# Performance work log

Measured on AMD Instinct MI355X. Metric: run time of the kernel, lower is better.

Reference implementation:

```python
import jax, jax.numpy as jnp
import numpy as np

B, T, D_MODEL, H, DH = 4, 2048, 768, 12, 64


def _rope_tables(T, dh):
    # standard rotary frequencies, (T, dh//2)
    inv_freq = 1.0 / (10000.0 ** (np.arange(0, dh, 2, dtype=np.float32) / dh))
    t = np.arange(T, dtype=np.float32)
    ang = np.outer(t, inv_freq)  # (T, dh//2)
    return jnp.asarray(np.cos(ang)), jnp.asarray(np.sin(ang))


def setup_inputs() -> dict:
    key = jax.random.key(0)
    ks = jax.random.split(key, 5)
    scale = 1.0 / np.sqrt(D_MODEL)
    x = jax.random.normal(ks[0], (B, T, D_MODEL), dtype=jnp.float32)
    wq = jax.random.normal(ks[1], (D_MODEL, D_MODEL), dtype=jnp.float32) * scale
    wk = jax.random.normal(ks[2], (D_MODEL, D_MODEL), dtype=jnp.float32) * scale
    wv = jax.random.normal(ks[3], (D_MODEL, D_MODEL), dtype=jnp.float32) * scale
    wo = jax.random.normal(ks[4], (D_MODEL, D_MODEL), dtype=jnp.float32) * scale
    rope_cos, rope_sin = _rope_tables(T, DH)
    return {"x": x, "rope_cos": rope_cos, "rope_sin": rope_sin,
            "wq": wq, "wk": wk, "wv": wv, "wo": wo}


def _apply_rope(x, cos, sin):
    # x: (B, H, T, DH), cos/sin: (T, DH//2) -> interleaved rotation
    t = x.shape[2]
    c = cos[:t][None, None]  # (1,1,T,DH//2)
    s = sin[:t][None, None]
    x1 = x[..., ::2]
    x2 = x[..., 1::2]
    return jnp.stack([x1 * c - x2 * s, x1 * s + x2 * c], axis=-1).reshape(x.shape)


def reference(x, rope_cos, rope_sin, wq, wk, wv, wo):
    b, t, _ = x.shape
    # Linear (torch nn.Linear: y = x @ W.T), split heads -> (B,H,T,DH)
    q = (x @ wq.T).reshape(b, t, H, DH).transpose(0, 2, 1, 3)
    k = (x @ wk.T).reshape(b, t, H, DH).transpose(0, 2, 1, 3)
    v = (x @ wv.T).reshape(b, t, H, DH).transpose(0, 2, 1, 3)
    q = _apply_rope(q, rope_cos, rope_sin)
    k = _apply_rope(k, rope_cos, rope_sin)
    scores = jnp.einsum("bhqd,bhkd->bhqk", q, k) * (DH ** -0.5)
    causal = jnp.tril(jnp.ones((t, t), dtype=bool))  # (T,T)
    scores = jnp.where(causal[None, None], scores, -jnp.inf)
    attn = jax.nn.softmax(scores, axis=-1)
    out = jnp.einsum("bhqk,bhkd->bhqd", attn, v)
    out = out.transpose(0, 2, 1, 3).reshape(b, t, H * DH)
    return out @ wo.T
```

## Files before the change

kernel.cpp:

```cpp
#include <hip/hip_runtime.h>
#include <hip/hip_bf16.h>
#include <math.h>

#define B_ 4
#define T_ 2048
#define DM 768
#define H_ 12
#define DH 64

typedef __attribute__((ext_vector_type(4))) float f32x4;
typedef __attribute__((ext_vector_type(8))) short s16x8;

typedef const __attribute__((address_space(1))) void* gas1_t;
typedef __attribute__((address_space(3))) void* las3_t;

__device__ __forceinline__ ushort f2b(float f) {
  union { float f; unsigned u; } v; v.f = f;
  unsigned u = v.u;
  u += 0x7fffu + ((u >> 16) & 1u);
  return (ushort)(u >> 16);
}
__device__ __forceinline__ float b2f(ushort b) {
  union { unsigned u; float f; } v; v.u = ((unsigned)b) << 16;
  return v.f;
}
__device__ __forceinline__ unsigned cvt_pk_bf16(float lo, float hi) {
  unsigned r;
  asm("v_cvt_pk_bf16_f32 %0, %1, %2" : "=v"(r) : "v"(lo), "v"(hi));
  return r;
}

__global__ void cvt_all(const float* __restrict__ x,
                        const float* __restrict__ wq, const float* __restrict__ wk,
                        const float* __restrict__ wv, const float* __restrict__ wo,
                        const float* __restrict__ rc, const float* __restrict__ rs,
                        ushort* __restrict__ xb, ushort* __restrict__ wqkv,
                        ushort* __restrict__ wob, float2* __restrict__ cs2) {
  const int bid = blockIdx.x, t = threadIdx.x;
  if (bid < 6144) {
    int i = bid * 256 + t;
    float4 v = ((const float4*)x)[i];
    ushort4 o;
    o.x = f2b(v.x); o.y = f2b(v.y); o.z = f2b(v.z); o.w = f2b(v.w);
    ((ushort4*)xb)[i] = o;
  } else if (bid < 8448) {
    int i = (bid - 6144) * 256 + t;
    int which = i / 147456, j = i - which * 147456;
    const float* src = which == 0 ? wq : which == 1 ? wk : which == 2 ? wv : wo;
    ushort* dst = which < 3 ? wqkv + (size_t)which * 589824 : wob;
    float4 v = ((const float4*)src)[j];
    ushort4 o;
    o.x = f2b(v.x); o.y = f2b(v.y); o.z = f2b(v.z); o.w = f2b(v.w);
    ((ushort4*)dst)[j] = o;
  } else {
    int i = (bid - 8448) * 256 + t;
    cs2[i] = make_float2(rc[i], rs[i]);
  }
}

__global__ __launch_bounds__(256, 3) void gemm_qkv(
    const ushort* __restrict__ A, const ushort* __restrict__ Bw,
    const float2* __restrict__ cs2,
    ushort* __restrict__ Qb, ushort* __restrict__ Kb, ushort* __restrict__ Vt) {
  const int K = 768;
  __shared__ ushort As[128 * 64];
  __shared__ ushort Bs[128 * 64];
  const int bid = blockIdx.x;
  const int xcd = bid & 7;
  const int jj = bid >> 3;
  const int mloc = jj / 18, nn0 = jj - mloc * 18;
  const int m0 = (xcd * 8 + mloc) * 128, n0 = nn0 * 128;
  const int tid = threadIdx.x;
  const int wave = tid >> 6, lane = tid & 63;
  const int wm = (wave >> 1) * 64, wn = (wave & 1) * 64;
  const int quad = lane >> 4, l16 = lane & 15;
  const int tr = tid >> 3;
  const int scb = (tid & 7) ^ (tr & 7);
  const int swz = l16 & 7;

  f32x4 acc[4][4] = {};

  const ushort* ga = A + (size_t)(m0 + tr) * K + scb * 8;
  const ushort* gb = Bw + (size_t)(n0 + tr) * K + scb * 8;

  for (int k0 = 0; k0 < K; k0 += 64) {
#pragma unroll
    for (int p = 0; p < 4; p++) {
      __builtin_amdgcn_global_load_lds((gas1_t)(ga + (size_t)(p * 32) * K + k0),
                                       (las3_t)(As + p * 2048 + tid * 8), 16, 0, 0);
      __builtin_amdgcn_global_load_lds((gas1_t)(gb + (size_t)(p * 32) * K + k0),
                                       (las3_t)(Bs + p * 2048 + tid * 8), 16, 0, 0);
    }
    __syncthreads();
#pragma unroll
    for (int kk = 0; kk < 2; kk++) {
      s16x8 af[4], bf[4];
#pragma unroll
      for (int i = 0; i < 4; i++) {
        const ushort* ar = As + (wm + i * 16 + l16) * 64;
        af[i] = *(const s16x8*)(ar + (((kk * 4 + quad) ^ swz) * 8));
        const ushort* br = Bs + (wn + i * 16 + l16) * 64;
        bf[i] = *(const s16x8*)(br + (((kk * 4 + quad) ^ swz) * 8));
      }
#pragma unroll
      for (int i = 0; i < 4; i++)
#pragma unroll
        for (int n = 0; n < 4; n++)
          acc[i][n] = __builtin_amdgcn_mfma_f32_16x16x32_bf16(af[i], bf[n], acc[i][n], 0, 0, 0);
    }
    __syncthreads();
  }

  const int sec = n0 / 768;
  if (sec < 2) {
    ushort* dst = sec == 0 ? Qb : Kb;
#pragma unroll
    for (int i = 0; i < 4; i++) {
      int row0 = m0 + wm + i * 16 + quad * 4;
#pragma unroll
      for (int nt = 0; nt < 4; nt++) {
        int col = n0 + wn + nt * 16 + l16;
        int nv = col - sec * 768;
        int h = nv >> 6, d = nv & 63;
        int ip = (d >> 1) & 31;
        float sgn = (d & 1) ? 1.f : -1.f;
#pragma unroll
        for (int r = 0; r < 4; r++) {
          int rrow = row0 + r;
          int t = rrow & (T_ - 1), bb = rrow >> 11;
          float v = acc[i][nt][r];
          float partner = __shfl_xor(v, 1);
          float2 cs = cs2[t * 32 + ip];
          float out = fmaf(v, cs.x, sgn * partner * cs.y);
          dst[((size_t)(bb * H_ + h) * T_ + t) * DH + d] = f2b(out);
        }
      }
    }
  } else {
#pragma unroll
    for (int i = 0; i < 4; i++) {
      int row0 = m0 + wm + i * 16 + quad * 4;
      int t0 = row0 & (T_ - 1), b = row0 >> 11;
#pragma unroll
      for (int nt = 0; nt < 4; nt++) {
        int col = n0 + wn + nt * 16 + l16;
        int nv = col - 1536;
        int h = nv >> 6, d = nv & 63;
        ushort4 pk;
        pk.x = f2b(acc[i][nt][0]); pk.y = f2b(acc[i][nt][1]);
        pk.z = f2b(acc[i][nt][2]); pk.w = f2b(acc[i][nt][3]);
        *(ushort4*)(Vt + ((size_t)(b * H_ + h) * DH + d) * T_ + t0) = pk;
      }
    }
  }
}

__global__ __launch_bounds__(256, 3) void gemm_out(
    const ushort* __restrict__ A, const ushort* __restrict__ Bw, float* __restrict__ C) {
  const int K = 768, N = 768;
  __shared__ ushort As[128 * 64];
  __shared__ ushort Bs[128 * 64];
  const int bid = blockIdx.x;
  const int xcd = bid & 7;
  const int jj = bid >> 3;
  const int mloc = jj / 6, nn0 = jj - mloc * 6;
  const int m0 = (xcd * 8 + mloc) * 128, n0 = nn0 * 128;
  const int tid = threadIdx.x;
  const int wave = tid >> 6, lane = tid & 63;
  const int wm = (wave >> 1) * 64, wn = (wave & 1) * 64;
  const int quad = lane >> 4, l16 = lane & 15;
  const int tr = tid >> 3;
  const int scb = (tid & 7) ^ (tr & 7);
  const int swz = l16 & 7;

  f32x4 acc[4][4] = {};

  const ushort* ga = A + (size_t)(m0 + tr) * K + scb * 8;
  const ushort* gb = Bw + (size_t)(n0 + tr) * K + scb * 8;

  for (int k0 = 0; k0 < K; k0 += 64) {
#pragma unroll
    for (int p = 0; p < 4; p++) {
      __builtin_amdgcn_global_load_lds((gas1_t)(ga + (size_t)(p * 32) * K + k0),
                                       (las3_t)(As + p * 2048 + tid * 8), 16, 0, 0);
      __builtin_amdgcn_global_load_lds((gas1_t)(gb + (size_t)(p * 32) * K + k0),
                                       (las3_t)(Bs + p * 2048 + tid * 8), 16, 0, 0);
    }
    __syncthreads();
#pragma unroll
    for (int kk = 0; kk < 2; kk++) {
      s16x8 af[4], bf[4];
#pragma unroll
      for (int i = 0; i < 4; i++) {
        const ushort* ar = As + (wm + i * 16 + l16) * 64;
        af[i] = *(const s16x8*)(ar + (((kk * 4 + quad) ^ swz) * 8));
        const ushort* br = Bs + (wn + i * 16 + l16) * 64;
        bf[i] = *(const s16x8*)(br + (((kk * 4 + quad) ^ swz) * 8));
      }
#pragma unroll
      for (int i = 0; i < 4; i++)
#pragma unroll
        for (int n = 0; n < 4; n++)
          acc[i][n] = __builtin_amdgcn_mfma_f32_16x16x32_bf16(af[i], bf[n], acc[i][n], 0, 0, 0);
    }
    __syncthreads();
  }

#pragma unroll
  for (int i = 0; i < 4; i++) {
    int row = m0 + wm + i * 16 + quad * 4;
#pragma unroll
    for (int n = 0; n < 4; n++) {
      int col = n0 + wn + n * 16 + l16;
#pragma unroll
      for (int r = 0; r < 4; r++)
        C[(size_t)(row + r) * N + col] = acc[i][n][r];
    }
  }
}

#define EXP2SCALE 0.18033688f
#define EXP2OFF  17.312340f
__global__ __launch_bounds__(256, 3) void attn(const ushort* __restrict__ Qb, const ushort* __restrict__ Kb,
                                               const ushort* __restrict__ Vt, ushort* __restrict__ Ob) {
  const int bh = blockIdx.x;
  const int p = blockIdx.y;
  const int tid = threadIdx.x, wave = tid >> 6, lane = tid & 63;
  const int quad = lane >> 4, l16 = lane & 15;
  const int b = bh / H_, h = bh % H_;
  const ushort* Qp = Qb + (size_t)bh * T_ * DH;
  const ushort* Kp = Kb + (size_t)bh * T_ * DH;
  const ushort* Vp = Vt + (size_t)bh * DH * T_;

  __shared__ ushort Ks[2][64 * 64];
  __shared__ ushort Vs[2][64 * 64];
  __shared__ ushort P[4][16][72];

  const int myTile = (wave < 2) ? p : (31 - p);
  const int qbase0 = myTile * 64 + (wave & 1) * 32;

  s16x8 aq[2][2];
#pragma unroll
  for (int m = 0; m < 2; m++) {
    const ushort* qp = Qp + (size_t)(qbase0 + m * 16 + l16) * DH + quad * 8;
    aq[m][0] = *(const s16x8*)qp;
    aq[m][1] = *(const s16x8*)(qp + 32);
  }
  f32x4 o[2][4] = {};
  float rsum[2] = {0.f, 0.f};

  const int ntile = 32 - p;
  const int srow = tid >> 3;
  const int scbK = (tid & 7) ^ (srow & 7);
  const int swz = (l16 & 7);

  {
    const int kv0 = 0;
    __builtin_amdgcn_global_load_lds((gas1_t)(Kp + (size_t)(kv0 + srow) * DH + scbK * 8),
                                     (las3_t)(Ks[0] + tid * 8), 16, 0, 0);
    __builtin_amdgcn_global_load_lds((gas1_t)(Kp + (size_t)(kv0 + srow + 32) * DH + scbK * 8),
                                     (las3_t)(Ks[0] + 2048 + tid * 8), 16, 0, 0);
    __builtin_amdgcn_global_load_lds((gas1_t)(Vp + (size_t)srow * T_ + kv0 + scbK * 8),
                                     (las3_t)(Vs[0] + tid * 8), 16, 0, 0);
    __builtin_amdgcn_global_load_lds((gas1_t)(Vp + (size_t)(srow + 32) * T_ + kv0 + scbK * 8),
                                     (las3_t)(Vs[0] + 2048 + tid * 8), 16, 0, 0);
  }

  for (int c = 0; c < ntile; c++) {
    const int kv0 = c * 64;
    const int cur = c & 1;
    __syncthreads();
    if (c + 1 < ntile) {
      const int kv1 = kv0 + 64, nxt = cur ^ 1;
      __builtin_amdgcn_global_load_lds((gas1_t)(Kp + (size_t)(kv1 + srow) * DH + scbK * 8),
                                       (las3_t)(Ks[nxt] + tid * 8), 16, 0, 0);
      __builtin_amdgcn_global_load_lds((gas1_t)(Kp + (size_t)(kv1 + srow + 32) * DH + scbK * 8),
                                       (las3_t)(Ks[nxt] + 2048 + tid * 8), 16, 0, 0);
      __builtin_amdgcn_global_load_lds((gas1_t)(Vp + (size_t)srow * T_ + kv1 + scbK * 8),
                                       (las3_t)(Vs[nxt] + tid * 8), 16, 0, 0);
      __builtin_amdgcn_global_load_lds((gas1_t)(Vp + (size_t)(srow + 32) * T_ + kv1 + scbK * 8),
                                       (las3_t)(Vs[nxt] + 2048 + tid * 8), 16, 0, 0);
    }

    if (kv0 <= qbase0 + 31) {
      s16x8 kf[4][2];
#pragma unroll
      for (int nt = 0; nt < 4; nt++) {
        const ushort* kr = Ks[cur] + (nt * 16 + l16) * 64;
        kf[nt][0] = *(const s16x8*)(kr + ((quad ^ swz) * 8));
        kf[nt][1] = *(const s16x8*)(kr + (((4 + quad) ^ swz) * 8));
      }
      s16x8 bv[4][2];
#pragma unroll
      for (int dt = 0; dt < 4; dt++) {
        const ushort* vr = Vs[cur] + (dt * 16 + l16) * 64;
        bv[dt][0] = *(const s16x8*)(vr + ((quad ^ swz) * 8));
        bv[dt][1] = *(const s16x8*)(vr + (((4 + quad) ^ swz) * 8));
      }

#pragma unroll
      for (int m = 0; m < 2; m++) {
        const int qb = qbase0 + m * 16;
        if (kv0 > qb + 15) continue;
        f32x4 s[4] = {};
#pragma unroll
        for (int nt = 0; nt < 4; nt++) {
          s[nt] = __builtin_amdgcn_mfma_f32_16x16x32_bf16(kf[nt][0], aq[m][0], s[nt], 0, 0, 0);
          s[nt] = __builtin_amdgcn_mfma_f32_16x16x32_bf16(kf[nt][1], aq[m][1], s[nt], 0, 0, 0);
        }
        if (kv0 + 63 <= qb) {
#pragma unroll
          for (int nt = 0; nt < 4; nt++) {
            float p0 = __builtin_amdgcn_exp2f(fmaf(s[nt][0], EXP2SCALE, -EXP2OFF));
            float p1 = __builtin_amdgcn_exp2f(fmaf(s[nt][1], EXP2SCALE, -EXP2OFF));
            float p2 = __builtin_amdgcn_exp2f(fmaf(s[nt][2], EXP2SCALE, -EXP2OFF));
            float p3 = __builtin_amdgcn_exp2f(fmaf(s[nt][3], EXP2SCALE, -EXP2OFF));
            rsum[m] += (p0 + p1) + (p2 + p3);
            uint2 pk;
            pk.x = cvt_pk_bf16(p0, p1);
            pk.y = cvt_pk_bf16(p2, p3);
            *(uint2*)&P[wave][l16][nt * 16 + quad * 4] = pk;
          }
        } else {
          int qi = qb + l16;
#pragma unroll
          for (int nt = 0; nt < 4; nt++) {
            int kvb = kv0 + nt * 16 + quad * 4;
            float pv[4];
#pragma unroll
            for (int r = 0; r < 4; r++)
              pv[r] = (kvb + r <= qi) ? __builtin_amdgcn_exp2f(fmaf(s[nt][r], EXP2SCALE, -EXP2OFF)) : 0.f;
            rsum[m] += (pv[0] + pv[1]) + (pv[2] + pv[3]);
            uint2 pk;
            pk.x = cvt_pk_bf16(pv[0], pv[1]);
            pk.y = cvt_pk_bf16(pv[2], pv[3]);
            *(uint2*)&P[wave][l16][nt * 16 + quad * 4] = pk;
          }
        }
        s16x8 ap0 = *(const s16x8*)&P[wave][l16][quad * 8];
        s16x8 ap1 = *(const s16x8*)&P[wave][l16][32 + quad * 8];
#pragma unroll
        for (int dt = 0; dt < 4; dt++) {
          o[m][dt] = __builtin_amdgcn_mfma_f32_16x16x32_bf16(ap0, bv[dt][0], o[m][dt], 0, 0, 0);
          o[m][dt] = __builtin_amdgcn_mfma_f32_16x16x32_bf16(ap1, bv[dt][1], o[m][dt], 0, 0, 0);
        }
      }
    }
  }
#pragma unroll
  for (int m = 0; m < 2; m++) {
    rsum[m] += __shfl_xor(rsum[m], 16);
    rsum[m] += __shfl_xor(rsum[m], 32);
  }
#pragma unroll
  for (int m = 0; m < 2; m++)
#pragma unroll
    for (int r = 0; r < 4; r++) {
      float inv = 1.0f / __shfl(rsum[m], quad * 4 + r);
      int q = qbase0 + m * 16 + quad * 4 + r;
#pragma unroll
      for (int dt = 0; dt < 4; dt++)
        Ob[(size_t)(b * T_ + q) * DM + h * 64 + dt * 16 + l16] = f2b(o[m][dt][r] * inv);
    }
}

extern "C" void kernel_launch(void* const* d_in, const int* in_sizes, int n_in,
                              void* d_out, int out_size, void* d_ws, size_t ws_size,
                              hipStream_t stream) {
  const float* x = (const float*)d_in[0];
  const float* rc = (const float*)d_in[1];
  const float* rs = (const float*)d_in[2];
  const float* wq = (const float*)d_in[3];
  const float* wk = (const float*)d_in[4];
  const float* wv = (const float*)d_in[5];
  const float* wo = (const float*)d_in[6];

  char* ws = (char*)d_ws;
  ushort* xb   = (ushort*)(ws);
  ushort* wqkv = (ushort*)(ws + 12582912);
  ushort* wob  = (ushort*)(ws + 16121856);
  float2* cs2  = (float2*)(ws + 17301504);
  ushort* Qb   = (ushort*)(ws + 17825792);
  ushort* Kb   = (ushort*)(ws + 30408704);
  ushort* Vt   = (ushort*)(ws + 42991616);
  ushort* Ob   = (ushort*)(ws + 55574528);

  cvt_all<<<8704, 256, 0, stream>>>(x, wq, wk, wv, wo, rc, rs, xb, wqkv, wob, cs2);

  gemm_qkv<<<1152, 256, 0, stream>>>(xb, wqkv, cs2, Qb, Kb, Vt);

  attn<<<dim3(48, 16), 256, 0, stream>>>(Qb, Kb, Vt, Ob);

  gemm_out<<<384, 256, 0, stream>>>(Ob, wob, (float*)d_out);
}
```

Baseline: 195.5 us.

## Retile QKV and output GEMMs, swizzle attention P buffer, vectorize output stores

The QKV projection GEMM now uses 128x192 tiles, giving 768 blocks instead of 1152 and more reuse of each loaded A tile. The output GEMM uses 128x96 tiles, giving 512 blocks instead of 384 so more CUs are filled. In attention the padded P scratch is replaced by an XOR-swizzled 64-wide layout, and the PV MFMA operands are swapped so each lane holds four consecutive head dims and can write Ob with packed ushort4 stores instead of scalar stores. The larger QKV tile raises accumulator register and LDS use, which may lower occupancy.

```diff
diff --git a/kernel.cpp b/kernel.cpp
--- a/kernel.cpp
+++ b/kernel.cpp
@@ -19,10 +19,6 @@
   unsigned u = v.u;
   u += 0x7fffu + ((u >> 16) & 1u);
   return (ushort)(u >> 16);
-}
-__device__ __forceinline__ float b2f(ushort b) {
-  union { unsigned u; float f; } v; v.u = ((unsigned)b) << 16;
-  return v.f;
 }
 __device__ __forceinline__ unsigned cvt_pk_bf16(float lo, float hi) {
   unsigned r;
@@ -64,48 +60,52 @@
     ushort* __restrict__ Qb, ushort* __restrict__ Kb, ushort* __restrict__ Vt) {
   const int K = 768;
   __shared__ ushort As[128 * 64];
-  __shared__ ushort Bs[128 * 64];
+  __shared__ ushort Bs[192 * 64];
   const int bid = blockIdx.x;
   const int xcd = bid & 7;
   const int jj = bid >> 3;
-  const int mloc = jj / 18, nn0 = jj - mloc * 18;
-  const int m0 = (xcd * 8 + mloc) * 128, n0 = nn0 * 128;
+  const int mloc = jj / 12, nn0 = jj - mloc * 12;
+  const int m0 = (xcd * 8 + mloc) * 128, n0 = nn0 * 192;
   const int tid = threadIdx.x;
   const int wave = tid >> 6, lane = tid & 63;
-  const int wm = (wave >> 1) * 64, wn = (wave & 1) * 64;
+  const int wm = (wave >> 1) * 64, wn = (wave & 1) * 96;
   const int quad = lane >> 4, l16 = lane & 15;
   const int tr = tid >> 3;
   const int scb = (tid & 7) ^ (tr & 7);
   const int swz = l16 & 7;
 
-  f32x4 acc[4][4] = {};
+  f32x4 acc[4][6] = {};
 
   const ushort* ga = A + (size_t)(m0 + tr) * K + scb * 8;
   const ushort* gb = Bw + (size_t)(n0 + tr) * K + scb * 8;
 
   for (int k0 = 0; k0 < K; k0 += 64) {
 #pragma unroll
-    for (int p = 0; p < 4; p++) {
+    for (int p = 0; p < 4; p++)
       __builtin_amdgcn_global_load_lds((gas1_t)(ga + (size_t)(p * 32) * K + k0),
                                        (las3_t)(As + p * 2048 + tid * 8), 16, 0, 0);
+#pragma unroll
+    for (int p = 0; p < 6; p++)
       __builtin_amdgcn_global_load_lds((gas1_t)(gb + (size_t)(p * 32) * K + k0),
                                        (las3_t)(Bs + p * 2048 + tid * 8), 16, 0, 0);
-    }
     __syncthreads();
 #pragma unroll
     for (int kk = 0; kk < 2; kk++) {
-      s16x8 af[4], bf[4];
+      s16x8 af[4], bf[6];
 #pragma unroll
       for (int i = 0; i < 4; i++) {
         const ushort* ar = As + (wm + i * 16 + l16) * 64;
         af[i] = *(const s16x8*)(ar + (((kk * 4 + quad) ^ swz) * 8));
-        const ushort* br = Bs + (wn + i * 16 + l16) * 64;
-        bf[i] = *(const s16x8*)(br + (((kk * 4 + quad) ^ swz) * 8));
+      }
+#pragma unroll
+      for (int n = 0; n < 6; n++) {
+        const ushort* br = Bs + (wn + n * 16 + l16) * 64;
+        bf[n] = *(const s16x8*)(br + (((kk * 4 + quad) ^ swz) * 8));
       }
 #pragma unroll
       for (int i = 0; i < 4; i++)
 #pragma unroll
-        for (int n = 0; n < 4; n++)
+        for (int n = 0; n < 6; n++)
           acc[i][n] = __builtin_amdgcn_mfma_f32_16x16x32_bf16(af[i], bf[n], acc[i][n], 0, 0, 0);
     }
     __syncthreads();
@@ -118,7 +118,7 @@
     for (int i = 0; i < 4; i++) {
       int row0 = m0 + wm + i * 16 + quad * 4;
 #pragma unroll
-      for (int nt = 0; nt < 4; nt++) {
+      for (int nt = 0; nt < 6; nt++) {
         int col = n0 + wn + nt * 16 + l16;
         int nv = col - sec * 768;
         int h = nv >> 6, d = nv & 63;
@@ -142,7 +142,7 @@
       int row0 = m0 + wm + i * 16 + quad * 4;
       int t0 = row0 & (T_ - 1), b = row0 >> 11;
 #pragma unroll
-      for (int nt = 0; nt < 4; nt++) {
+      for (int nt = 0; nt < 6; nt++) {
         int col = n0 + wn + nt * 16 + l16;
         int nv = col - 1536;
         int h = nv >> 6, d = nv & 63;
@@ -159,48 +159,52 @@
     const ushort* __restrict__ A, const ushort* __restrict__ Bw, float* __restrict__ C) {
   const int K = 768, N = 768;
   __shared__ ushort As[128 * 64];
-  __shared__ ushort Bs[128 * 64];
+  __shared__ ushort Bs[96 * 64];
   const int bid = blockIdx.x;
   const int xcd = bid & 7;
   const int jj = bid >> 3;
-  const int mloc = jj / 6, nn0 = jj - mloc * 6;
-  const int m0 = (xcd * 8 + mloc) * 128, n0 = nn0 * 128;
+  const int mloc = jj >> 3, nn0 = jj & 7;
+  const int m0 = (xcd * 8 + mloc) * 128, n0 = nn0 * 96;
   const int tid = threadIdx.x;
   const int wave = tid >> 6, lane = tid & 63;
-  const int wm = (wave >> 1) * 64, wn = (wave & 1) * 64;
+  const int wm = (wave >> 1) * 64, wn = (wave & 1) * 48;
   const int quad = lane >> 4, l16 = lane & 15;
   const int tr = tid >> 3;
   const int scb = (tid & 7) ^ (tr & 7);
   const int swz = l16 & 7;
 
-  f32x4 acc[4][4] = {};
+  f32x4 acc[4][3] = {};
 
   const ushort* ga = A + (size_t)(m0 + tr) * K + scb * 8;
   const ushort* gb = Bw + (size_t)(n0 + tr) * K + scb * 8;
 
   for (int k0 = 0; k0 < K; k0 += 64) {
 #pragma unroll
-    for (int p = 0; p < 4; p++) {
+    for (int p = 0; p < 4; p++)
       __builtin_amdgcn_global_load_lds((gas1_t)(ga + (size_t)(p * 32) * K + k0),
                                        (las3_t)(As + p * 2048 + tid * 8), 16, 0, 0);
+#pragma unroll
+    for (int p = 0; p < 3; p++)
       __builtin_amdgcn_global_load_lds((gas1_t)(gb + (size_t)(p * 32) * K + k0),
                                        (las3_t)(Bs + p * 2048 + tid * 8), 16, 0, 0);
-    }
     __syncthreads();
 #pragma unroll
     for (int kk = 0; kk < 2; kk++) {
-      s16x8 af[4], bf[4];
+      s16x8 af[4], bf[3];
 #pragma unroll
       for (int i = 0; i < 4; i++) {
         const ushort* ar = As + (wm + i * 16 + l16) * 64;
         af[i] = *(const s16x8*)(ar + (((kk * 4 + quad) ^ swz) * 8));
-        const ushort* br = Bs + (wn + i * 16 + l16) * 64;
-        bf[i] = *(const s16x8*)(br + (((kk * 4 + quad) ^ swz) * 8));
+      }
+#pragma unroll
+      for (int n = 0; n < 3; n++) {
+        const ushort* br = Bs + (wn + n * 16 + l16) * 64;
+        bf[n] = *(const s16x8*)(br + (((kk * 4 + quad) ^ swz) * 8));
       }
 #pragma unroll
       for (int i = 0; i < 4; i++)
 #pragma unroll
-        for (int n = 0; n < 4; n++)
+        for (int n = 0; n < 3; n++)
           acc[i][n] = __builtin_amdgcn_mfma_f32_16x16x32_bf16(af[i], bf[n], acc[i][n], 0, 0, 0);
     }
     __syncthreads();
@@ -210,7 +214,7 @@
   for (int i = 0; i < 4; i++) {
     int row = m0 + wm + i * 16 + quad * 4;
 #pragma unroll
-    for (int n = 0; n < 4; n++) {
+    for (int n = 0; n < 3; n++) {
       int col = n0 + wn + n * 16 + l16;
 #pragma unroll
       for (int r = 0; r < 4; r++)
@@ -234,7 +238,7 @@
 
   __shared__ ushort Ks[2][64 * 64];
   __shared__ ushort Vs[2][64 * 64];
-  __shared__ ushort P[4][16][72];
+  __shared__ ushort P[4][16][64];
 
   const int myTile = (wave < 2) ? p : (31 - p);
   const int qbase0 = myTile * 64 + (wave & 1) * 32;
@@ -253,6 +257,7 @@
   const int srow = tid >> 3;
   const int scbK = (tid & 7) ^ (srow & 7);
   const int swz = (l16 & 7);
+  const int psw = swz << 3;
 
   {
     const int kv0 = 0;
@@ -316,10 +321,9 @@
             float p2 = __builtin_amdgcn_exp2f(fmaf(s[nt][2], EXP2SCALE, -EXP2OFF));
             float p3 = __builtin_amdgcn_exp2f(fmaf(s[nt][3], EXP2SCALE, -EXP2OFF));
             rsum[m] += (p0 + p1) + (p2 + p3);
-            uint2 pk;
-            pk.x = cvt_pk_bf16(p0, p1);
-            pk.y = cvt_pk_bf16(p2, p3);
-            *(uint2*)&P[wave][l16][nt * 16 + quad * 4] = pk;
+            int sc = (nt * 16 + quad * 4) ^ psw;
+            *(unsigned*)&P[wave][l16][sc] = cvt_pk_bf16(p0, p1);
+            *(unsigned*)&P[wave][l16][sc + 2] = cvt_pk_bf16(p2, p3);
           }
         } else {
           int qi = qb + l16;
@@ -331,18 +335,17 @@
             for (int r = 0; r < 4; r++)
               pv[r] = (kvb + r <= qi) ? __builtin_amdgcn_exp2f(fmaf(s[nt][r], EXP2SCALE, -EXP2OFF)) : 0.f;
             rsum[m] += (pv[0] + pv[1]) + (pv[2] + pv[3]);
-            uint2 pk;
-            pk.x = cvt_pk_bf16(pv[0], pv[1]);
-            pk.y = cvt_pk_bf16(pv[2], pv[3]);
-            *(uint2*)&P[wave][l16][nt * 16 + quad * 4] = pk;
+            int sc = (nt * 16 + quad * 4) ^ psw;
+            *(unsigned*)&P[wave][l16][sc] = cvt_pk_bf16(pv[0], pv[1]);
+            *(unsigned*)&P[wave][l16][sc + 2] = cvt_pk_bf16(pv[2], pv[3]);
           }
         }
-        s16x8 ap0 = *(const s16x8*)&P[wave][l16][quad * 8];
-        s16x8 ap1 = *(const s16x8*)&P[wave][l16][32 + quad * 8];
+        s16x8 ap0 = *(const s16x8*)&P[wave][l16][(quad * 8) ^ psw];
+        s16x8 ap1 = *(const s16x8*)&P[wave][l16][(32 + quad * 8) ^ psw];
 #pragma unroll
         for (int dt = 0; dt < 4; dt++) {
-          o[m][dt] = __builtin_amdgcn_mfma_f32_16x16x32_bf16(ap0, bv[dt][0], o[m][dt], 0, 0, 0);
-          o[m][dt] = __builtin_amdgcn_mfma_f32_16x16x32_bf16(ap1, bv[dt][1], o[m][dt], 0, 0, 0);
+          o[m][dt] = __builtin_amdgcn_mfma_f32_16x16x32_bf16(bv[dt][0], ap0, o[m][dt], 0, 0, 0);
+          o[m][dt] = __builtin_amdgcn_mfma_f32_16x16x32_bf16(bv[dt][1], ap1, o[m][dt], 0, 0, 0);
         }
       }
     }
@@ -353,15 +356,18 @@
     rsum[m] += __shfl_xor(rsum[m], 32);
   }
 #pragma unroll
-  for (int m = 0; m < 2; m++)
-#pragma unroll
-    for (int r = 0; r < 4; r++) {
-      float inv = 1.0f / __shfl(rsum[m], quad * 4 + r);
-      int q = qbase0 + m * 16 + quad * 4 + r;
-#pragma unroll
-      for (int dt = 0; dt < 4; dt++)
-        Ob[(size_t)(b * T_ + q) * DM + h * 64 + dt * 16 + l16] = f2b(o[m][dt][r] * inv);
-    }
+  for (int m = 0; m < 2; m++) {
+    float inv = 1.0f / rsum[m];
+    int q = qbase0 + m * 16 + l16;
+    size_t base = (size_t)(b * T_ + q) * DM + h * 64 + quad * 4;
+#pragma unroll
+    for (int dt = 0; dt < 4; dt++) {
+      ushort4 pk4;
+      pk4.x = f2b(o[m][dt][0] * inv); pk4.y = f2b(o[m][dt][1] * inv);
+      pk4.z = f2b(o[m][dt][2] * inv); pk4.w = f2b(o[m][dt][3] * inv);
+      *(ushort4*)&Ob[base + dt * 16] = pk4;
+    }
+  }
 }
 
 extern "C" void kernel_launch(void* const* d_in, const int* in_sizes, int n_in,
@@ -387,9 +393,9 @@
 
   cvt_all<<<8704, 256, 0, stream>>>(x, wq, wk, wv, wo, rc, rs, xb, wqkv, wob, cs2);
 
-  gemm_qkv<<<1152, 256, 0, stream>>>(xb, wqkv, cs2, Qb, Kb, Vt);
+  gemm_qkv<<<768, 256, 0, stream>>>(xb, wqkv, cs2, Qb, Kb, Vt);
 
   attn<<<dim3(48, 16), 256, 0, stream>>>(Qb, Kb, Vt, Ob);
 
-  gemm_out<<<384, 256, 0, stream>>>(Ob, wob, (float*)d_out);
-}
+  gemm_out<<<512, 256, 0, stream>>>(Ob, wob, (float*)d_out);
+}
```

Result: slower. 209.2 us (+7.0%).
